# Optimization experiments

Hardware: AMD Instinct MI355X
Metric: run time of the kernel (lower is better)

## Reference

```python
import jax, jax.numpy as jnp
import numpy as np
from jax import lax

NUM_THRESH = 100  # torch.linspace(0, 1, steps=100)


def _neighbor_max(lab):
    # 4-connectivity neighbor max with zero padding; lab: [T, B, H, W] int32
    up = jnp.pad(lab[:, :, 1:, :], ((0, 0), (0, 0), (0, 1), (0, 0)))
    dn = jnp.pad(lab[:, :, :-1, :], ((0, 0), (0, 0), (1, 0), (0, 0)))
    lf = jnp.pad(lab[:, :, :, 1:], ((0, 0), (0, 0), (0, 0), (0, 1)))
    rt = jnp.pad(lab[:, :, :, :-1], ((0, 0), (0, 0), (0, 0), (1, 0)))
    return jnp.maximum(jnp.maximum(up, dn), jnp.maximum(lf, rt))


def count_components(binz):
    # binz: [T, B, H, W] float {0,1}. Parallel CCL via iterative max-label
    # propagation (the vectorized equivalent of the source's per-pixel DFS).
    T, B, H, W = binz.shape
    ids = (jnp.arange(H * W, dtype=jnp.int32) + 1).reshape(H, W)  # unique id per pixel
    mask = binz > 0
    lab0 = jnp.where(mask, ids, 0).astype(jnp.int32)

    def body(_, lab):
        return jnp.where(mask, jnp.maximum(lab, _neighbor_max(lab)), 0)

    lab = lax.fori_loop(0, 2 * (H + W), body, lab0)
    # one representative pixel per component keeps its own id (the max id)
    roots = jnp.logical_and(lab == ids, mask)
    return jnp.sum(roots.astype(jnp.float32), axis=(2, 3))  # [T, B]


def euler_number(binz):
    # euler = #pixels - #4-connected edges  (faithful to compute_euler_number)
    px = jnp.sum(binz, axis=(2, 3))
    ev = jnp.sum(binz[:, :, :-1, :] * binz[:, :, 1:, :], axis=(2, 3))
    eh = jnp.sum(binz[:, :, :, :-1] * binz[:, :, :, 1:], axis=(2, 3))
    return px - (ev + eh)  # [T, B]


def compute_betti_numbers(prob, thresholds):
    # prob: [B, H, W] -> betti: [B, T, 2] with (b0, b1), b1 = b0 - euler
    binz = (prob[None] > thresholds[:, None, None, None]).astype(jnp.float32)
    b0 = count_components(binz)          # [T, B]
    b1 = b0 - euler_number(binz)          # [T, B]
    return jnp.stack([b0, b1], axis=-1).transpose(1, 0, 2)  # [B, T, 2]


def setup_inputs() -> dict:
    key = jax.random.key(0)
    k1, k2 = jax.random.split(key)
    three_class_prob = jax.random.uniform(k1, (8, 3, 64, 64), dtype=jnp.float32)
    gt_betti = jax.random.randint(k2, (8, 3, NUM_THRESH, 2), 0, 10, dtype=jnp.int32)
    return {"three_class_prob": three_class_prob, "gt_betti": gt_betti}


def reference(three_class_prob, gt_betti):
    thresholds = jnp.linspace(0.0, 1.0, NUM_THRESH, dtype=jnp.float32)
    inside_betti = compute_betti_numbers(three_class_prob[:, 0], thresholds)
    boundary_betti = compute_betti_numbers(three_class_prob[:, 1], thresholds)
    union_betti = inside_betti  # source uses channel 0 slice for 'union' too
    gt = gt_betti.astype(jnp.float32)
    err = (jnp.sum(jnp.abs(inside_betti - gt[:, 0]), axis=(1, 2))
           + jnp.sum(jnp.abs(boundary_betti - gt[:, 1]), axis=(1, 2))
           + jnp.sum(jnp.abs(union_betti - gt[:, 2]), axis=(1, 2)))
    return err  # [B] per-image topology error
```

## Files before the change

kernel.cpp:

```cpp
#include <hip/hip_runtime.h>

#define NT 100

__device__ __forceinline__ int find_root(int* P, int x) {
    int p = P[x];
    while (p != x) {
        int gp = P[p];
        P[x] = gp;
        x = gp;
        p = P[x];
    }
    return x;
}

__device__ __forceinline__ void unite(int* P, int a, int b) {
    a = find_root(P, a);
    b = find_root(P, b);
    while (a != b) {
        if (a < b) { int t = a; a = b; b = t; }
        int old = atomicCAS(&P[a], a, b);
        if (old == a) return;
        a = find_root(P, old);
        b = find_root(P, b);
    }
}

__global__ __launch_bounds__(256)
void betti_partial(const float* __restrict__ prob,
                   const int*  __restrict__ gt,
                   int* __restrict__ part)
{
    __shared__ int P[2048];
    __shared__ int bL[3][64];
    __shared__ int bR[3][64];
    __shared__ unsigned long long wred[4];

    const int bid = blockIdx.x;
    const int t   = bid % NT;
    const int cb  = bid / NT;
    const int c   = cb & 1;
    const int b   = cb >> 1;

    const float thr = (float)t * (1.0f / 99.0f);
    const float* img = prob + (size_t)(b * 3 + c) * 4096;

    const int tid  = threadIdx.x;
    const int h    = tid >> 6;
    const int lane = tid & 63;

    const float4* rp = (const float4*)(img + (lane << 6) + (h << 4));
    unsigned int m = 0;
    #pragma unroll
    for (int q = 0; q < 4; ++q) {
        float4 v = rp[q];
        m |= (unsigned)(v.x > thr) << (4 * q + 0);
        m |= (unsigned)(v.y > thr) << (4 * q + 1);
        m |= (unsigned)(v.z > thr) << (4 * q + 2);
        m |= (unsigned)(v.w > thr) << (4 * q + 3);
    }

    #pragma unroll
    for (int k = 0; k < 8; ++k) {
        int s = ((h * 8 + k) << 6) | lane;
        P[s] = s;
    }

    const unsigned um = m & 0xFFFFu;
    unsigned up        = (unsigned)__shfl_up((int)um, 1, 64);
    unsigned starts    = um & ~(um << 1) & 0xFFFFu;
    unsigned starts_up = (unsigned)__shfl_up((int)starts, 1, 64);
    if (lane == 0) { up = 0u; starts_up = 0u; }

    const int px    = __popc(um);
    const int eh    = __popc(um & (um >> 1));
    const int ev    = __popc(um & up);
    const int nruns = __popc(starts);

    if (h < 3)
        bL[h][lane] = ((um >> 15) & 1u) ? (((h * 8 + (nruns - 1)) << 6) | lane) : -1;
    if (h > 0)
        bR[h - 1][lane] = (um & 1u) ? (((h * 8) << 6) | lane) : -1;

    __syncthreads();

    unsigned ov = um & up;
    unsigned ss = ov & ~(ov << 1) & 0xFFFFu;
    while (ss) {
        int j = __ffs(ss) - 1;
        ss &= ss - 1;
        unsigned le = (2u << j) - 1;
        int kc = __popc(starts    & le) - 1;
        int ku = __popc(starts_up & le) - 1;
        unite(P, ((h * 8 + kc) << 6) | lane, ((h * 8 + ku) << 6) | (lane - 1));
    }

    int ehx = 0;
    if (h < 3) {
        int l = bL[h][lane], r = bR[h][lane];
        if (l >= 0 && r >= 0) { ehx = 1; unite(P, l, r); }
    }
    __syncthreads();

    int selfc = 0;
    #pragma unroll
    for (int k = 0; k < 8; ++k) {
        int s = ((h * 8 + k) << 6) | lane;
        selfc += (P[s] == s) ? 1 : 0;
    }
    const int roots = selfc - (8 - nruns);

    unsigned long long pk = (unsigned long long)px
                          | ((unsigned long long)(eh + ehx) << 16)
                          | ((unsigned long long)ev         << 32)
                          | ((unsigned long long)roots      << 48);
    #pragma unroll
    for (int o = 32; o > 0; o >>= 1)
        pk += __shfl_down(pk, o, 64);
    if (lane == 0) wred[h] = pk;
    __syncthreads();

    if (tid == 0) {
        unsigned long long s = wred[0] + wred[1] + wred[2] + wred[3];
        const int spx = (int)(s         & 0xffff);
        const int seh = (int)((s >> 16) & 0xffff);
        const int sev = (int)((s >> 32) & 0xffff);
        const int b0  = (int)((s >> 48) & 0xffff);
        const int euler = spx - (seh + sev);
        const int b1 = b0 - euler;

        int contrib = 0, d;
        if (c == 0) {
            const int* g0 = gt + (((size_t)b * 3 + 0) * NT + t) * 2;
            const int* g2 = gt + (((size_t)b * 3 + 2) * NT + t) * 2;
            d = b0 - g0[0]; contrib += d < 0 ? -d : d;
            d = b1 - g0[1]; contrib += d < 0 ? -d : d;
            d = b0 - g2[0]; contrib += d < 0 ? -d : d;
            d = b1 - g2[1]; contrib += d < 0 ? -d : d;
        } else {
            const int* g1 = gt + (((size_t)b * 3 + 1) * NT + t) * 2;
            d = b0 - g1[0]; contrib += d < 0 ? -d : d;
            d = b1 - g1[1]; contrib += d < 0 ? -d : d;
        }
        part[bid] = contrib;
    }
}

__global__ __launch_bounds__(256)
void betti_reduce(const int* __restrict__ part, float* __restrict__ out) {
    __shared__ int wsum[4];
    const int b = blockIdx.x;
    const int tid = threadIdx.x;
    int v = (tid < 200) ? part[b * 200 + tid] : 0;
    #pragma unroll
    for (int o = 32; o > 0; o >>= 1) v += __shfl_down(v, o, 64);
    if ((tid & 63) == 0) wsum[tid >> 6] = v;
    __syncthreads();
    if (tid == 0)
        out[b] = (float)(wsum[0] + wsum[1] + wsum[2] + wsum[3]);
}

extern "C" void kernel_launch(void* const* d_in, const int* in_sizes, int n_in,
                              void* d_out, int out_size, void* d_ws, size_t ws_size,
                              hipStream_t stream) {
    const float* prob = (const float*)d_in[0];
    const int*   gt   = (const int*)d_in[1];
    float* out = (float*)d_out;
    int* part = (int*)d_ws;

    const int nblocks = 8 * 2 * NT;
    betti_partial<<<nblocks, 256, 0, stream>>>(prob, gt, part);
    betti_reduce<<<8, 256, 0, stream>>>(part, out);
}
```

Baseline: 19.39 us.

## Count components via successful merges and move block finalization into the reduce kernel

Component count is now the number of row runs minus the number of successful union operations, so the final root scan over shared memory is dropped. The first barrier before the vertical unions is removed, since those only touch each wave's own rows. Per-wave packed counters are written straight to the workspace, and the cross-wave sum and GT comparison move into the second kernel, which drops the trailing barriers and the single-thread epilogue. The bit fields are packed more tightly, and correctness depends on each union returning 1 exactly once per real merge.

```diff
diff --git a/kernel.cpp b/kernel.cpp
--- a/kernel.cpp
+++ b/kernel.cpp
@@ -1,5 +1,6 @@
 #include <hip/hip_runtime.h>
 
+typedef unsigned long long ull;
 #define NT 100
 
 __device__ __forceinline__ int find_root(int* P, int x) {
@@ -13,36 +14,33 @@
     return x;
 }
 
-__device__ __forceinline__ void unite(int* P, int a, int b) {
+__device__ __forceinline__ int unite(int* P, int a, int b) {
     a = find_root(P, a);
     b = find_root(P, b);
     while (a != b) {
         if (a < b) { int t = a; a = b; b = t; }
         int old = atomicCAS(&P[a], a, b);
-        if (old == a) return;
+        if (old == a) return 1;
         a = find_root(P, old);
         b = find_root(P, b);
     }
+    return 0;
 }
 
 __global__ __launch_bounds__(256)
 void betti_partial(const float* __restrict__ prob,
-                   const int*  __restrict__ gt,
-                   int* __restrict__ part)
+                   ull* __restrict__ ws)
 {
     __shared__ int P[2048];
     __shared__ int bL[3][64];
     __shared__ int bR[3][64];
-    __shared__ unsigned long long wred[4];
 
     const int bid = blockIdx.x;
     const int t   = bid % NT;
     const int cb  = bid / NT;
-    const int c   = cb & 1;
-    const int b   = cb >> 1;
 
     const float thr = (float)t * (1.0f / 99.0f);
-    const float* img = prob + (size_t)(b * 3 + c) * 4096;
+    const float* img = prob + (size_t)((cb >> 1) * 3 + (cb & 1)) * 4096;
 
     const int tid  = threadIdx.x;
     const int h    = tid >> 6;
@@ -72,7 +70,7 @@
     if (lane == 0) { up = 0u; starts_up = 0u; }
 
     const int px    = __popc(um);
-    const int eh    = __popc(um & (um >> 1));
+    int       eh    = __popc(um & (um >> 1));
     const int ev    = __popc(um & up);
     const int nruns = __popc(starts);
 
@@ -81,8 +79,7 @@
     if (h > 0)
         bR[h - 1][lane] = (um & 1u) ? (((h * 8) << 6) | lane) : -1;
 
-    __syncthreads();
-
+    int merges = 0;
     unsigned ov = um & up;
     unsigned ss = ov & ~(ov << 1) & 0xFFFFu;
     while (ss) {
@@ -91,44 +88,52 @@
         unsigned le = (2u << j) - 1;
         int kc = __popc(starts    & le) - 1;
         int ku = __popc(starts_up & le) - 1;
-        unite(P, ((h * 8 + kc) << 6) | lane, ((h * 8 + ku) << 6) | (lane - 1));
+        merges += unite(P, ((h * 8 + kc) << 6) | lane, ((h * 8 + ku) << 6) | (lane - 1));
     }
 
-    int ehx = 0;
+    __syncthreads();
+
     if (h < 3) {
         int l = bL[h][lane], r = bR[h][lane];
-        if (l >= 0 && r >= 0) { ehx = 1; unite(P, l, r); }
+        if (l >= 0 && r >= 0) { eh++; merges += unite(P, l, r); }
     }
-    __syncthreads();
 
-    int selfc = 0;
-    #pragma unroll
-    for (int k = 0; k < 8; ++k) {
-        int s = ((h * 8 + k) << 6) | lane;
-        selfc += (P[s] == s) ? 1 : 0;
-    }
-    const int roots = selfc - (8 - nruns);
-
-    unsigned long long pk = (unsigned long long)px
-                          | ((unsigned long long)(eh + ehx) << 16)
-                          | ((unsigned long long)ev         << 32)
-                          | ((unsigned long long)roots      << 48);
+    ull pk = (ull)px
+           | ((ull)eh     << 13)
+           | ((ull)ev     << 25)
+           | ((ull)nruns  << 37)
+           | ((ull)merges << 49);
     #pragma unroll
     for (int o = 32; o > 0; o >>= 1)
         pk += __shfl_down(pk, o, 64);
-    if (lane == 0) wred[h] = pk;
-    __syncthreads();
 
-    if (tid == 0) {
-        unsigned long long s = wred[0] + wred[1] + wred[2] + wred[3];
-        const int spx = (int)(s         & 0xffff);
-        const int seh = (int)((s >> 16) & 0xffff);
-        const int sev = (int)((s >> 32) & 0xffff);
-        const int b0  = (int)((s >> 48) & 0xffff);
-        const int euler = spx - (seh + sev);
-        const int b1 = b0 - euler;
+    if (lane == 0) ws[(size_t)bid * 4 + h] = pk;
+}
 
-        int contrib = 0, d;
+__global__ __launch_bounds__(256)
+void betti_final(const ull* __restrict__ ws,
+                 const int* __restrict__ gt,
+                 float* __restrict__ out)
+{
+    __shared__ int wsum[4];
+    const int b = blockIdx.x;
+    const int tid = threadIdx.x;
+
+    int contrib = 0;
+    if (tid < 200) {
+        const ull* p = ws + (size_t)(b * 200 + tid) * 4;
+        ull s = p[0] + p[1] + p[2] + p[3];
+        const int px = (int)( s        & 0x1FFF);
+        const int eh = (int)((s >> 13) & 0xFFF);
+        const int ev = (int)((s >> 25) & 0xFFF);
+        const int nr = (int)((s >> 37) & 0xFFF);
+        const int mg = (int)((s >> 49) & 0xFFF);
+        const int b0 = nr - mg;
+        const int b1 = b0 - (px - (eh + ev));
+
+        const int c = tid / 100;
+        const int t = tid - c * 100;
+        int d;
         if (c == 0) {
             const int* g0 = gt + (((size_t)b * 3 + 0) * NT + t) * 2;
             const int* g2 = gt + (((size_t)b * 3 + 2) * NT + t) * 2;
@@ -141,19 +146,11 @@
             d = b0 - g1[0]; contrib += d < 0 ? -d : d;
             d = b1 - g1[1]; contrib += d < 0 ? -d : d;
         }
-        part[bid] = contrib;
     }
-}
 
-__global__ __launch_bounds__(256)
-void betti_reduce(const int* __restrict__ part, float* __restrict__ out) {
-    __shared__ int wsum[4];
-    const int b = blockIdx.x;
-    const int tid = threadIdx.x;
-    int v = (tid < 200) ? part[b * 200 + tid] : 0;
     #pragma unroll
-    for (int o = 32; o > 0; o >>= 1) v += __shfl_down(v, o, 64);
-    if ((tid & 63) == 0) wsum[tid >> 6] = v;
+    for (int o = 32; o > 0; o >>= 1) contrib += __shfl_down(contrib, o, 64);
+    if ((tid & 63) == 0) wsum[tid >> 6] = contrib;
     __syncthreads();
     if (tid == 0)
         out[b] = (float)(wsum[0] + wsum[1] + wsum[2] + wsum[3]);
@@ -165,9 +162,9 @@
     const float* prob = (const float*)d_in[0];
     const int*   gt   = (const int*)d_in[1];
     float* out = (float*)d_out;
-    int* part = (int*)d_ws;
+    ull* ws = (ull*)d_ws;
 
     const int nblocks = 8 * 2 * NT;
-    betti_partial<<<nblocks, 256, 0, stream>>>(prob, gt, part);
-    betti_reduce<<<8, 256, 0, stream>>>(part, out);
+    betti_partial<<<nblocks, 256, 0, stream>>>(prob, ws);
+    betti_final<<<8, 256, 0, stream>>>(ws, gt, out);
 }
```

Measured after the change: 19.30 us. No clear change (-0.5%).
